# Kernel tuning notes

Hardware: AMD Instinct MI355X
Metric: run time of the kernel (lower is better)

The kernel has to match this reference:

```python
import jax, jax.numpy as jnp
import numpy as np
from jax import lax

N_HEADS = 12
HEAD_DIM = 64
ALPHA = 4.0  # spikingjelly surrogate.Sigmoid default alpha
EPS = 1e-5   # BatchNorm1d default eps

@jax.custom_vjp
def _heaviside(v):
    return (v >= 0.0).astype(v.dtype)

def _heaviside_fwd(v):
    return _heaviside(v), v

def _heaviside_bwd(v, g):
    sg = jax.nn.sigmoid(ALPHA * v)
    return (g * ALPHA * sg * (1.0 - sg),)

_heaviside.defvjp(_heaviside_fwd, _heaviside_bwd)

def if_node(x):
    """Multi-step IFNode (v_threshold=1, hard reset to 0), scan over leading T dim."""
    def step(v, xt):
        v = v + xt                      # integrate
        s = _heaviside(v - 1.0)         # fire
        v = (1.0 - s) * v               # hard reset: spiked neurons -> 0
        return v, s
    _, spikes = lax.scan(step, jnp.zeros_like(x[0]), x)
    return spikes

def bn1d(x):
    """Fresh (training-mode) BatchNorm1d over (T, S, D) with channels=S;
    affine weight=1, bias=0 at init, so pure normalization over axes (0,2)."""
    mean = x.mean(axis=(0, 2), keepdims=True)
    var = x.var(axis=(0, 2), keepdims=True)  # biased variance, as torch BN uses
    return (x - mean) * lax.rsqrt(var + EPS)

def setup_inputs() -> dict:
    key = jax.random.key(0)
    ks = jax.random.split(key, 5)
    T, S, D = 4, 2048, 768
    x = jax.random.normal(ks[0], (T, S, D), dtype=jnp.float32)
    scale = 0.02
    wq = jax.random.normal(ks[1], (D, D), dtype=jnp.float32) * scale
    wk = jax.random.normal(ks[2], (D, D), dtype=jnp.float32) * scale
    wv = jax.random.normal(ks[3], (D, D), dtype=jnp.float32) * scale
    wo = jax.random.normal(ks[4], (D, D), dtype=jnp.float32) * scale
    return {"x": x, "wq": wq, "wk": wk, "wv": wv, "wo": wo, "cur_pos": S}

def reference(x, wq, wk, wv, wo, cur_pos):
    T, S, D = x.shape
    tmp = if_node(x)                    # init_spike
    Q = tmp @ wq
    V = tmp @ wv
    K = tmp @ wk
    Q = if_node(bn1d(Q))                # spike_q(bnq(Q))
    V = if_node(bn1d(V))                # spike_v(bnv(V))
    K = if_node(bn1d(K))                # spike_k(bnk(K))
    # (T, S, H, hd) -> (T, H, S, hd)
    Qh = Q.reshape(T, S, N_HEADS, HEAD_DIM).transpose(0, 2, 1, 3)
    Vh = V.reshape(T, S, N_HEADS, HEAD_DIM).transpose(0, 2, 1, 3)
    Kh = K.reshape(T, S, N_HEADS, HEAD_DIM).transpose(0, 2, 1, 3)
    QK = (Qh * Kh).sum(axis=2, keepdims=True)   # (T, H, 1, hd)
    QK = if_node(QK)                    # talking_heads
    QKV = Vh * QK                       # (T, H, S, hd)
    QKV = QKV.transpose(0, 2, 1, 3).reshape(T, S, D)
    return bn1d(QKV @ wo)
```

## Files before the change

kernel.cpp:

```cpp
#include <hip/hip_runtime.h>

#define T_ 4
#define S_ 2048
#define D_ 768
#define SD_ (S_ * D_)
#define TSD_ (T_ * SD_)
#define H_ 12
#define HD_ 64
#define PLANE_BYTES 2359296u

typedef int int32x4 __attribute__((ext_vector_type(4)));

__device__ __forceinline__ void cp16(unsigned char* lds, const unsigned char* g) {
    __builtin_amdgcn_global_load_lds(
        (const __attribute__((address_space(1))) unsigned int*)g,
        (__attribute__((address_space(3))) unsigned int*)lds, 16, 0, 0);
}

__device__ __forceinline__ size_t frag_addr(int m, int d) {
    return ((size_t)(m >> 4) * 12 + (d >> 6)) * 1024 +
           (size_t)(((d >> 4) & 3) * 256 + (m & 15) * 16 + (d & 15));
}

__global__ __launch_bounds__(256) void k_prep_all(const float* __restrict__ wq,
                                                  const float* __restrict__ wk,
                                                  const float* __restrict__ wv,
                                                  const float* __restrict__ wo,
                                                  const float* __restrict__ x,
                                                  unsigned char* __restrict__ Bp,
                                                  unsigned char* __restrict__ Sx) {
    __shared__ unsigned char wl[4096];
    int tid = threadIdx.x;
    if (blockIdx.y < 4) {
        const float* W = (blockIdx.y == 0) ? wq : (blockIdx.y == 1) ? wk
                       : (blockIdx.y == 2) ? wv : wo;
        unsigned char* out = Bp + (size_t)blockIdx.y * PLANE_BYTES;
        int c = blockIdx.x;
        int kb = c % 12;
        int nbg = c / 12;
        int k_loc = tid >> 2;
        int n_base = (tid & 3) * 4;
        float4 w4 = *(const float4*)(
            W + (size_t)(kb * 64 + k_loc) * D_ + nbg * 16 + n_base);
        float wsv[4] = {w4.x, w4.y, w4.z, w4.w};
#pragma unroll
        for (int j = 0; j < 4; j++) {
            int n_loc = n_base + j;
            int u = (int)rintf(wsv[j] * 1073741824.0f);
#pragma unroll
            for (int p = 0; p < 4; p++) {
                wl[p * 1024 + (n_loc + 16 * (k_loc >> 4)) * 16 + (k_loc & 15)] =
                    (unsigned char)(u & 255);
                u = (u + 128) >> 8;
            }
        }
        __syncthreads();
        int p = tid >> 6;
        int lane = tid & 63;
        uint4 val = *(const uint4*)&wl[p * 1024 + lane * 16];
        *(uint4*)(out + (size_t)((p * 48 + nbg) * 12 + kb) * 1024 + lane * 16) =
            val;
    } else {
        if (blockIdx.x >= 384) return;
        int gid = blockIdx.x * 256 + tid;
        int s = gid / 48;
        int d0 = (gid % 48) * 16;
        double v[16];
#pragma unroll
        for (int j = 0; j < 16; j++) v[j] = 0.0;
#pragma unroll
        for (int t = 0; t < T_; t++) {
            union { uint4 u; unsigned char b[16]; } sp;
#pragma unroll
            for (int q = 0; q < 4; q++) {
                float4 xt = *(const float4*)(
                    x + (size_t)t * SD_ + (size_t)s * D_ + d0 + q * 4);
                float xs[4] = {xt.x, xt.y, xt.z, xt.w};
#pragma unroll
                for (int j = 0; j < 4; j++) {
                    int jj = q * 4 + j;
                    v[jj] += (double)xs[j];
                    unsigned char ss = (v[jj] >= 1.0) ? 1 : 0;
                    sp.b[jj] = ss;
                    if (ss) v[jj] = 0.0;
                }
            }
            *(uint4*)(Sx + frag_addr(t * S_ + s, d0)) = sp.u;
        }
    }
}

__global__ __launch_bounds__(256, 2) void k_gemm_i8(
    const unsigned char* __restrict__ A,
    const unsigned char* __restrict__ Bp,
    const unsigned char* __restrict__ Ms,
    float* __restrict__ C0, float* __restrict__ C1, float* __restrict__ C2,
    int bzoff) {
    int z = blockIdx.z;
    const unsigned char* B = Bp + (size_t)(bzoff + z) * PLANE_BYTES;
    float* C = (z == 0) ? C0 : (z == 1) ? C1 : C2;

    __shared__ __align__(16) unsigned char bsm[2 * 16384];

    int tid = threadIdx.x;
    int lane = tid & 63;
    int w = tid >> 6;
    int wm = w >> 1;
    int wn = w & 1;
    int row0 = blockIdx.x * 128;
    int tI = row0 >> 11;
    int n0 = blockIdx.y * 64;
    int nbg0 = blockIdx.y * 4;
    int col = lane & 15;
    int quad = lane >> 4;

    int32x4 zerov = {0, 0, 0, 0};
    int32x4 acc[4][2][4];
#pragma unroll
    for (int mb = 0; mb < 4; mb++)
#pragma unroll
        for (int nb = 0; nb < 2; nb++)
#pragma unroll
            for (int p = 0; p < 4; p++) acc[mb][nb][p] = zerov;

    const unsigned char* Ab =
        A + (size_t)((row0 >> 4) + wm * 4) * 12 * 1024 + lane * 16;

    auto stageB = [&](int buf, int kb) {
        unsigned char* bb = bsm + buf * 16384;
#pragma unroll
        for (int qi = 0; qi < 4; qi++) {
            int q = w * 4 + qi;
            int p = q >> 2, nb = q & 3;
            cp16(bb + q * 1024,
                 B + (size_t)((p * 48 + nbg0 + nb) * 12 + kb) * 1024 + lane * 16);
        }
    };

    int32x4 a[2][4];
#pragma unroll
    for (int mb = 0; mb < 4; mb++)
        a[0][mb] = *(const int32x4*)(Ab + (size_t)(mb * 12) * 1024);
    stageB(0, 0);
    __syncthreads();

    for (int kb = 0; kb < 12; kb++) {
        int cur = kb & 1;
        if (kb < 11) {
            stageB(1 - cur, kb + 1);
#pragma unroll
            for (int mb = 0; mb < 4; mb++)
                a[1 - cur][mb] = *(const int32x4*)(
                    Ab + (size_t)(mb * 12 + kb + 1) * 1024);
        }
        int32x4 af[4];
#pragma unroll
        for (int mb = 0; mb < 4; mb++) af[mb] = a[cur][mb];
        if (Ms) {
            int32x4 mv = *(const int32x4*)(Ms + tI * D_ + kb * 64 + quad * 16);
#pragma unroll
            for (int mb = 0; mb < 4; mb++) af[mb] &= mv;
        }
        const unsigned char* bb = bsm + cur * 16384;
#pragma unroll
        for (int p = 0; p < 4; p++)
#pragma unroll
            for (int nb = 0; nb < 2; nb++) {
                int32x4 bf = *(const int32x4*)(
                    bb + (size_t)(p * 4 + wn * 2 + nb) * 1024 + lane * 16);
#pragma unroll
                for (int mb = 0; mb < 4; mb++)
                    acc[mb][nb][p] = __builtin_amdgcn_mfma_i32_16x16x64_i8(
                        af[mb], bf, acc[mb][nb][p], 0, 0, 0);
            }
        __syncthreads();
    }

#pragma unroll
    for (int mb = 0; mb < 4; mb++)
#pragma unroll
        for (int nb = 0; nb < 2; nb++)
#pragma unroll
            for (int r = 0; r < 4; r++) {
                long t = (long)acc[mb][nb][0][r] + ((long)acc[mb][nb][1][r] << 8)
                       + ((long)acc[mb][nb][2][r] << 16)
                       + ((long)acc[mb][nb][3][r] << 24);
                float v = (float)((double)t * (1.0 / 1073741824.0));
                int rr = row0 + wm * 64 + mb * 16 + quad * 4 + r;
                int cc = n0 + wn * 32 + nb * 16 + col;
                C[(size_t)rr * D_ + cc] = v;
            }
}

__global__ __launch_bounds__(256) void k_bn_if(const float* __restrict__ Qf,
                                               const float* __restrict__ Kf,
                                               const float* __restrict__ Vf,
                                               unsigned char* __restrict__ Qs,
                                               unsigned char* __restrict__ Ks,
                                               unsigned char* __restrict__ Vs) {
    int s = blockIdx.x;
    int y = blockIdx.y;
    const float* X = (y == 0) ? Qf : (y == 1) ? Kf : Vf;
    unsigned char* Sp = (y == 0) ? Qs : (y == 1) ? Ks : Vs;

    __shared__ float buf[T_][D_];
    __shared__ double red[16];
    __shared__ unsigned char spk[T_ * D_];

    int tid = threadIdx.x;
    double sum = 0.0, sumsq = 0.0;
#pragma unroll
    for (int t = 0; t < T_; t++) {
        for (int d = tid; d < D_; d += 256) {
            float v = X[(size_t)t * SD_ + (size_t)s * D_ + d];
            buf[t][d] = v;
            double dv = (double)v;
            sum += dv;
            sumsq += dv * dv;
        }
    }
#pragma unroll
    for (int off = 32; off > 0; off >>= 1) {
        sum += __shfl_down(sum, off);
        sumsq += __shfl_down(sumsq, off);
    }
    int lane = tid & 63, wv = tid >> 6;
    if (lane == 0) { red[wv] = sum; red[4 + wv] = sumsq; }
    __syncthreads();
    if (tid == 0) {
        double s4 = red[0] + red[1] + red[2] + red[3];
        double q4 = red[4] + red[5] + red[6] + red[7];
        double mean = s4 / 3072.0;
        double var = q4 / 3072.0 - mean * mean;
        red[8] = mean;
        red[9] = 1.0 / sqrt(var + 1e-5);
    }
    __syncthreads();
    double mean = red[8], rstd = red[9];
    for (int d = tid; d < D_; d += 256) {
        double v = 0.0;
#pragma unroll
        for (int t = 0; t < T_; t++) {
            double xn = ((double)buf[t][d] - mean) * rstd;
            v += xn;
            int sp = (v >= 1.0) ? 1 : 0;
            spk[t * D_ + d] = (unsigned char)sp;
            if (sp) v = 0.0;
        }
    }
    __syncthreads();
    if (tid < 192) {
        int tt = tid / 48, gg = tid % 48;
        uint4 val = *(const uint4*)&spk[tt * D_ + gg * 16];
        size_t dst = ((size_t)(tt * 128 + (s >> 4)) * 12 + (gg >> 2)) * 1024 +
                     (size_t)((gg & 3) * 256 + (s & 15) * 16);
        *(uint4*)(Sp + dst) = val;
    }
}

__global__ __launch_bounds__(256) void k_qk(const unsigned char* __restrict__ Qs,
                                            const unsigned char* __restrict__ Ks,
                                            float* __restrict__ QK) {
    int t = blockIdx.x / H_;
    int h = blockIdx.x % H_;
    int lane = threadIdx.x & 63;
    int w = threadIdx.x >> 6;
    size_t base = ((size_t)t * 128 * 12 + h) * 1024 + lane * 16;
    uint4 acc = make_uint4(0, 0, 0, 0);
    for (int c = w; c < 128; c += 4) {
        uint4 q = *(const uint4*)(Qs + base + (size_t)c * 12288);
        uint4 k = *(const uint4*)(Ks + base + (size_t)c * 12288);
        acc.x += q.x & k.x;
        acc.y += q.y & k.y;
        acc.z += q.z & k.z;
        acc.w += q.w & k.w;
    }
    __shared__ unsigned int part[4][64][4];
    part[w][lane][0] = acc.x;
    part[w][lane][1] = acc.y;
    part[w][lane][2] = acc.z;
    part[w][lane][3] = acc.w;
    __syncthreads();
    if (threadIdx.x < 64) {
        int quad = threadIdx.x >> 4;
        int rem = threadIdx.x & 15;
        int dw = rem >> 2;
        int b = rem & 3;
        unsigned int tot = 0;
#pragma unroll
        for (int ww = 0; ww < 4; ww++)
            for (int cc = 0; cc < 16; cc++)
                tot += (part[ww][quad * 16 + cc][dw] >> (8 * b)) & 255u;
        QK[t * D_ + h * HD_ + quad * 16 + dw * 4 + b] = (float)tot;
    }
}

__global__ __launch_bounds__(256) void k_if_qk(const float* __restrict__ QK,
                                               unsigned char* __restrict__ QKm) {
    int j = blockIdx.x * 256 + threadIdx.x;
    if (j >= D_) return;
    float v = 0.f;
#pragma unroll
    for (int t = 0; t < T_; t++) {
        v += QK[t * D_ + j];
        unsigned char sp = (v >= 1.0f) ? 1 : 0;
        QKm[t * D_ + j] = sp;
        if (sp) v = 0.f;
    }
}

__global__ __launch_bounds__(256) void k_bn_out(const float* __restrict__ Xin,
                                                float* __restrict__ out) {
    int s = blockIdx.x;
    __shared__ float buf[T_][D_];
    __shared__ double red[16];
    int tid = threadIdx.x;
    double sum = 0.0, sumsq = 0.0;
#pragma unroll
    for (int t = 0; t < T_; t++) {
        for (int d = tid; d < D_; d += 256) {
            float v = Xin[(size_t)t * SD_ + (size_t)s * D_ + d];
            buf[t][d] = v;
            double dv = (double)v;
            sum += dv;
            sumsq += dv * dv;
        }
    }
#pragma unroll
    for (int off = 32; off > 0; off >>= 1) {
        sum += __shfl_down(sum, off);
        sumsq += __shfl_down(sumsq, off);
    }
    int lane = tid & 63, wv = tid >> 6;
    if (lane == 0) { red[wv] = sum; red[4 + wv] = sumsq; }
    __syncthreads();
    if (tid == 0) {
        double s4 = red[0] + red[1] + red[2] + red[3];
        double q4 = red[4] + red[5] + red[6] + red[7];
        double mean = s4 / 3072.0;
        double var = q4 / 3072.0 - mean * mean;
        red[8] = mean;
        red[9] = 1.0 / sqrt(var + 1e-5);
    }
    __syncthreads();
    double mean = red[8], rstd = red[9];
    for (int d = tid; d < D_; d += 256) {
#pragma unroll
        for (int t = 0; t < T_; t++) {
            double v = (double)buf[t][d];
            out[(size_t)t * SD_ + (size_t)s * D_ + d] =
                (float)((v - mean) * rstd);
        }
    }
}

extern "C" void kernel_launch(void* const* d_in, const int* in_sizes, int n_in,
                              void* d_out, int out_size, void* d_ws,
                              size_t ws_size, hipStream_t stream) {
    const float* x  = (const float*)d_in[0];
    const float* wq = (const float*)d_in[1];
    const float* wk = (const float*)d_in[2];
    const float* wv = (const float*)d_in[3];
    const float* wo = (const float*)d_in[4];
    float* out = (float*)d_out;

    float* ws  = (float*)d_ws;
    float* Qf  = ws;
    float* Kf  = ws + (size_t)TSD_;
    float* Vf  = ws + (size_t)2 * TSD_;
    float* QK  = ws + (size_t)3 * TSD_;
    unsigned char* QKm = (unsigned char*)(QK + T_ * D_);
    unsigned char* Sx  = QKm + 4096;
    unsigned char* Ks  = Sx + (size_t)TSD_;
    unsigned char* Vs  = Ks + (size_t)TSD_;
    unsigned char* Bp  = Vs + (size_t)TSD_;
    unsigned char* Qs  = Sx;

    k_prep_all<<<dim3(576, 5), 256, 0, stream>>>(wq, wk, wv, wo, x, Bp, Sx);
    k_gemm_i8<<<dim3(64, 12, 3), 256, 0, stream>>>(Sx, Bp, nullptr,
                                                   Qf, Kf, Vf, 0);
    k_bn_if<<<dim3(S_, 3), 256, 0, stream>>>(Qf, Kf, Vf, Qs, Ks, Vs);
    k_qk<<<T_ * H_, 256, 0, stream>>>(Qs, Ks, QK);
    k_if_qk<<<3, 256, 0, stream>>>(QK, QKm);
    k_gemm_i8<<<dim3(64, 12, 1), 256, 0, stream>>>(Vs, Bp, QKm, Qf, Qf, Qf, 3);
    k_bn_out<<<S_, 256, 0, stream>>>(Qf, out);
}
```

Baseline: 246.5 us.

## Fuse BN+IF for Q/K/V with QK spike-mask reduction via atomicOr bitmask

Replaces the separate BN+IF, QK reduction and talking-heads IF kernels with one kernel per sequence position. It normalizes and spikes Q, K and V together and OR-reduces the Q&K spikes into a packed mask with atomicOr. This is exact because a count of at least 1 always fires the IF node and resets it. The change avoids writing and re-reading the Q/K spike planes, drops two launches, and zeroes the mask buffer inside the prep kernel. The int8 GEMM also stages two K-blocks per barrier, which halves the syncs but doubles LDS use. Its epilogue combines partial sums in double instead of int64.

```diff
diff --git a/kernel.cpp b/kernel.cpp
--- a/kernel.cpp
+++ b/kernel.cpp
@@ -28,7 +28,8 @@
                                                   const float* __restrict__ wo,
                                                   const float* __restrict__ x,
                                                   unsigned char* __restrict__ Bp,
-                                                  unsigned char* __restrict__ Sx) {
+                                                  unsigned char* __restrict__ Sx,
+                                                  unsigned int* __restrict__ QKp) {
     __shared__ unsigned char wl[4096];
     int tid = threadIdx.x;
     if (blockIdx.y < 4) {
@@ -61,7 +62,13 @@
         *(uint4*)(out + (size_t)((p * 48 + nbg) * 12 + kb) * 1024 + lane * 16) =
             val;
     } else {
-        if (blockIdx.x >= 384) return;
+        if (blockIdx.x >= 384) {
+            if (blockIdx.x < 432) {
+                int idx = (blockIdx.x - 384) * 256 + tid;
+                QKp[idx] = 0u;
+            }
+            return;
+        }
         int gid = blockIdx.x * 256 + tid;
         int s = gid / 48;
         int d0 = (gid % 48) * 16;
@@ -93,14 +100,15 @@
 __global__ __launch_bounds__(256, 2) void k_gemm_i8(
     const unsigned char* __restrict__ A,
     const unsigned char* __restrict__ Bp,
-    const unsigned char* __restrict__ Ms,
+    const unsigned int* __restrict__ Mp,
     float* __restrict__ C0, float* __restrict__ C1, float* __restrict__ C2,
     int bzoff) {
     int z = blockIdx.z;
     const unsigned char* B = Bp + (size_t)(bzoff + z) * PLANE_BYTES;
     float* C = (z == 0) ? C0 : (z == 1) ? C1 : C2;
 
-    __shared__ __align__(16) unsigned char bsm[2 * 16384];
+    __shared__ __align__(16) unsigned char bsm[2 * 32768];
+    __shared__ __align__(16) unsigned int maskw[192];
 
     int tid = threadIdx.x;
     int lane = tid & 63;
@@ -126,53 +134,67 @@
     const unsigned char* Ab =
         A + (size_t)((row0 >> 4) + wm * 4) * 12 * 1024 + lane * 16;
 
-    auto stageB = [&](int buf, int kb) {
-        unsigned char* bb = bsm + buf * 16384;
-#pragma unroll
-        for (int qi = 0; qi < 4; qi++) {
-            int q = w * 4 + qi;
-            int p = q >> 2, nb = q & 3;
-            cp16(bb + q * 1024,
-                 B + (size_t)((p * 48 + nbg0 + nb) * 12 + kb) * 1024 + lane * 16);
-        }
+    auto stageB = [&](int buf, int kb2) {
+        unsigned char* bb = bsm + buf * 32768;
+#pragma unroll
+        for (int kk = 0; kk < 2; kk++)
+#pragma unroll
+            for (int qi = 0; qi < 4; qi++) {
+                int q = w * 4 + qi;
+                int p = q >> 2, nb = q & 3;
+                cp16(bb + kk * 16384 + q * 1024,
+                     B + (size_t)((p * 48 + nbg0 + nb) * 12 + 2 * kb2 + kk) *
+                             1024 + lane * 16);
+            }
     };
 
+    stageB(0, 0);
+    if (Mp && tid < 192) {
+        unsigned int m = 0;
+#pragma unroll
+        for (int c = 0; c < 16; c++) m |= Mp[c * 768 + tI * 192 + tid];
+        maskw[tid] = m;
+    }
     int32x4 a[2][4];
 #pragma unroll
     for (int mb = 0; mb < 4; mb++)
         a[0][mb] = *(const int32x4*)(Ab + (size_t)(mb * 12) * 1024);
-    stageB(0, 0);
     __syncthreads();
 
-    for (int kb = 0; kb < 12; kb++) {
-        int cur = kb & 1;
-        if (kb < 11) {
-            stageB(1 - cur, kb + 1);
-#pragma unroll
-            for (int mb = 0; mb < 4; mb++)
-                a[1 - cur][mb] = *(const int32x4*)(
-                    Ab + (size_t)(mb * 12 + kb + 1) * 1024);
-        }
-        int32x4 af[4];
-#pragma unroll
-        for (int mb = 0; mb < 4; mb++) af[mb] = a[cur][mb];
-        if (Ms) {
-            int32x4 mv = *(const int32x4*)(Ms + tI * D_ + kb * 64 + quad * 16);
-#pragma unroll
-            for (int mb = 0; mb < 4; mb++) af[mb] &= mv;
-        }
-        const unsigned char* bb = bsm + cur * 16384;
-#pragma unroll
-        for (int p = 0; p < 4; p++)
-#pragma unroll
-            for (int nb = 0; nb < 2; nb++) {
-                int32x4 bf = *(const int32x4*)(
-                    bb + (size_t)(p * 4 + wn * 2 + nb) * 1024 + lane * 16);
+    for (int kb2 = 0; kb2 < 6; kb2++) {
+        int cur = kb2 & 1;
+        if (kb2 < 5) stageB(1 - cur, kb2 + 1);
+#pragma unroll
+        for (int kbh = 0; kbh < 2; kbh++) {
+            int kb = kb2 * 2 + kbh;
+            if (kb < 11) {
 #pragma unroll
                 for (int mb = 0; mb < 4; mb++)
-                    acc[mb][nb][p] = __builtin_amdgcn_mfma_i32_16x16x64_i8(
-                        af[mb], bf, acc[mb][nb][p], 0, 0, 0);
-            }
+                    a[(kb + 1) & 1][mb] = *(const int32x4*)(
+                        Ab + (size_t)(mb * 12 + kb + 1) * 1024);
+            }
+            int32x4 af[4];
+#pragma unroll
+            for (int mb = 0; mb < 4; mb++) af[mb] = a[kb & 1][mb];
+            if (Mp) {
+                int32x4 mv = *(const int32x4*)(
+                    (const unsigned char*)maskw + kb * 64 + quad * 16);
+#pragma unroll
+                for (int mb = 0; mb < 4; mb++) af[mb] &= mv;
+            }
+            const unsigned char* bb = bsm + cur * 32768 + kbh * 16384;
+#pragma unroll
+            for (int p = 0; p < 4; p++)
+#pragma unroll
+                for (int nb = 0; nb < 2; nb++) {
+                    int32x4 bf = *(const int32x4*)(
+                        bb + (size_t)(p * 4 + wn * 2 + nb) * 1024 + lane * 16);
+#pragma unroll
+                    for (int mb = 0; mb < 4; mb++)
+                        acc[mb][nb][p] = __builtin_amdgcn_mfma_i32_16x16x64_i8(
+                            af[mb], bf, acc[mb][nb][p], 0, 0, 0);
+                }
+        }
         __syncthreads();
     }
 
@@ -182,37 +204,111 @@
         for (int nb = 0; nb < 2; nb++)
 #pragma unroll
             for (int r = 0; r < 4; r++) {
-                long t = (long)acc[mb][nb][0][r] + ((long)acc[mb][nb][1][r] << 8)
-                       + ((long)acc[mb][nb][2][r] << 16)
-                       + ((long)acc[mb][nb][3][r] << 24);
-                float v = (float)((double)t * (1.0 / 1073741824.0));
+                double td = (double)acc[mb][nb][0][r]
+                          + 256.0 * (double)acc[mb][nb][1][r]
+                          + 65536.0 * (double)acc[mb][nb][2][r]
+                          + 16777216.0 * (double)acc[mb][nb][3][r];
+                float v = (float)(td * (1.0 / 1073741824.0));
                 int rr = row0 + wm * 64 + mb * 16 + quad * 4 + r;
                 int cc = n0 + wn * 32 + nb * 16 + col;
                 C[(size_t)rr * D_ + cc] = v;
             }
 }
 
-__global__ __launch_bounds__(256) void k_bn_if(const float* __restrict__ Qf,
-                                               const float* __restrict__ Kf,
-                                               const float* __restrict__ Vf,
-                                               unsigned char* __restrict__ Qs,
-                                               unsigned char* __restrict__ Ks,
-                                               unsigned char* __restrict__ Vs) {
+__global__ __launch_bounds__(256) void k_bnif_qk(const float* __restrict__ Qf,
+                                                 const float* __restrict__ Kf,
+                                                 const float* __restrict__ Vf,
+                                                 unsigned char* __restrict__ Vs,
+                                                 unsigned int* __restrict__ QKp) {
     int s = blockIdx.x;
-    int y = blockIdx.y;
-    const float* X = (y == 0) ? Qf : (y == 1) ? Kf : Vf;
-    unsigned char* Sp = (y == 0) ? Qs : (y == 1) ? Ks : Vs;
-
+    __shared__ float buf[3][T_][D_];
+    __shared__ double red[8];
+    __shared__ unsigned char spkV[T_ * D_];
+    __shared__ unsigned char spkA[T_ * D_];
+    __shared__ double stats[3][2];
+
+    int tid = threadIdx.x;
+    const float* Xs[3] = {Qf, Kf, Vf};
+#pragma unroll
+    for (int y = 0; y < 3; y++) {
+        double sum = 0.0, sumsq = 0.0;
+#pragma unroll
+        for (int t = 0; t < T_; t++) {
+            for (int d = tid; d < D_; d += 256) {
+                float v = Xs[y][(size_t)t * SD_ + (size_t)s * D_ + d];
+                buf[y][t][d] = v;
+                double dv = (double)v;
+                sum += dv;
+                sumsq += dv * dv;
+            }
+        }
+#pragma unroll
+        for (int off = 32; off > 0; off >>= 1) {
+            sum += __shfl_down(sum, off);
+            sumsq += __shfl_down(sumsq, off);
+        }
+        int lane = tid & 63, wv = tid >> 6;
+        if (lane == 0) { red[wv] = sum; red[4 + wv] = sumsq; }
+        __syncthreads();
+        if (tid == 0) {
+            double s4 = red[0] + red[1] + red[2] + red[3];
+            double q4 = red[4] + red[5] + red[6] + red[7];
+            double mean = s4 / 3072.0;
+            double var = q4 / 3072.0 - mean * mean;
+            stats[y][0] = mean;
+            stats[y][1] = 1.0 / sqrt(var + 1e-5);
+        }
+        __syncthreads();
+    }
+
+    for (int d = tid; d < D_; d += 256) {
+        unsigned char qs[T_], ks[T_];
+#pragma unroll
+        for (int y = 0; y < 3; y++) {
+            double mean = stats[y][0], rstd = stats[y][1];
+            double v = 0.0;
+#pragma unroll
+            for (int t = 0; t < T_; t++) {
+                double xn = ((double)buf[y][t][d] - mean) * rstd;
+                v += xn;
+                unsigned char sp = (v >= 1.0) ? 1 : 0;
+                if (y == 0) qs[t] = sp;
+                else if (y == 1) ks[t] = sp;
+                else spkV[t * D_ + d] = sp;
+                if (sp) v = 0.0;
+            }
+        }
+#pragma unroll
+        for (int t = 0; t < T_; t++) spkA[t * D_ + d] = qs[t] & ks[t];
+    }
+    __syncthreads();
+
+    if (tid < 192) {
+        int tt = tid / 48, gg = tid % 48;
+        uint4 val = *(const uint4*)&spkV[tt * D_ + gg * 16];
+        size_t dst = ((size_t)(tt * 128 + (s >> 4)) * 12 + (gg >> 2)) * 1024 +
+                     (size_t)((gg & 3) * 256 + (s & 15) * 16);
+        *(uint4*)(Vs + dst) = val;
+        unsigned int* dstq = QKp + (s & 15) * 768;
+#pragma unroll
+        for (int t = 0; t < T_; t++) {
+            unsigned int word = *(const unsigned int*)&spkA[t * D_ + tid * 4];
+            if (word) atomicOr(dstq + t * 192 + tid, word);
+        }
+    }
+}
+
+__global__ __launch_bounds__(256) void k_bn_out(const float* __restrict__ Xin,
+                                                float* __restrict__ out) {
+    int s = blockIdx.x;
     __shared__ float buf[T_][D_];
     __shared__ double red[16];
-    __shared__ unsigned char spk[T_ * D_];
-
     int tid = threadIdx.x;
     double sum = 0.0, sumsq = 0.0;
 #pragma unroll
     for (int t = 0; t < T_; t++) {
         for (int d = tid; d < D_; d += 256) {
-            float v = X[(size_t)t * SD_ + (size_t)s * D_ + d];
+            float v = Xin[(size_t)t * SD_ + (size_t)s * D_ + d];
             buf[t][d] = v;
             double dv = (double)v;
             sum += dv;
@@ -238,113 +334,6 @@
     __syncthreads();
     double mean = red[8], rstd = red[9];
     for (int d = tid; d < D_; d += 256) {
-        double v = 0.0;
-#pragma unroll
-        for (int t = 0; t < T_; t++) {
-            double xn = ((double)buf[t][d] - mean) * rstd;
-            v += xn;
-            int sp = (v >= 1.0) ? 1 : 0;
-            spk[t * D_ + d] = (unsigned char)sp;
-            if (sp) v = 0.0;
-        }
-    }
-    __syncthreads();
-    if (tid < 192) {
-        int tt = tid / 48, gg = tid % 48;
-        uint4 val = *(const uint4*)&spk[tt * D_ + gg * 16];
-        size_t dst = ((size_t)(tt * 128 + (s >> 4)) * 12 + (gg >> 2)) * 1024 +
-                     (size_t)((gg & 3) * 256 + (s & 15) * 16);
-        *(uint4*)(Sp + dst) = val;
-    }
-}
-
-__global__ __launch_bounds__(256) void k_qk(const unsigned char* __restrict__ Qs,
-                                            const unsigned char* __restrict__ Ks,
-                                            float* __restrict__ QK) {
-    int t = blockIdx.x / H_;
-    int h = blockIdx.x % H_;
-    int lane = threadIdx.x & 63;
-    int w = threadIdx.x >> 6;
-    size_t base = ((size_t)t * 128 * 12 + h) * 1024 + lane * 16;
-    uint4 acc = make_uint4(0, 0, 0, 0);
-    for (int c = w; c < 128; c += 4) {
-        uint4 q = *(const uint4*)(Qs + base + (size_t)c * 12288);
-        uint4 k = *(const uint4*)(Ks + base + (size_t)c * 12288);
-        acc.x += q.x & k.x;
-        acc.y += q.y & k.y;
-        acc.z += q.z & k.z;
-        acc.w += q.w & k.w;
-    }
-    __shared__ unsigned int part[4][64][4];
-    part[w][lane][0] = acc.x;
-    part[w][lane][1] = acc.y;
-    part[w][lane][2] = acc.z;
-    part[w][lane][3] = acc.w;
-    __syncthreads();
-    if (threadIdx.x < 64) {
-        int quad = threadIdx.x >> 4;
-        int rem = threadIdx.x & 15;
-        int dw = rem >> 2;
-        int b = rem & 3;
-        unsigned int tot = 0;
-#pragma unroll
-        for (int ww = 0; ww < 4; ww++)
-            for (int cc = 0; cc < 16; cc++)
-                tot += (part[ww][quad * 16 + cc][dw] >> (8 * b)) & 255u;
-        QK[t * D_ + h * HD_ + quad * 16 + dw * 4 + b] = (float)tot;
-    }
-}
-
-__global__ __launch_bounds__(256) void k_if_qk(const float* __restrict__ QK,
-                                               unsigned char* __restrict__ QKm) {
-    int j = blockIdx.x * 256 + threadIdx.x;
-    if (j >= D_) return;
-    float v = 0.f;
-#pragma unroll
-    for (int t = 0; t < T_; t++) {
-        v += QK[t * D_ + j];
-        unsigned char sp = (v >= 1.0f) ? 1 : 0;
-        QKm[t * D_ + j] = sp;
-        if (sp) v = 0.f;
-    }
-}
-
-__global__ __launch_bounds__(256) void k_bn_out(const float* __restrict__ Xin,
-                                                float* __restrict__ out) {
-    int s = blockIdx.x;
-    __shared__ float buf[T_][D_];
-    __shared__ double red[16];
-    int tid = threadIdx.x;
-    double sum = 0.0, sumsq = 0.0;
-#pragma unroll
-    for (int t = 0; t < T_; t++) {
-        for (int d = tid; d < D_; d += 256) {
-            float v = Xin[(size_t)t * SD_ + (size_t)s * D_ + d];
-            buf[t][d] = v;
-            double dv = (double)v;
-            sum += dv;
-            sumsq += dv * dv;
-        }
-    }
-#pragma unroll
-    for (int off = 32; off > 0; off >>= 1) {
-        sum += __shfl_down(sum, off);
-        sumsq += __shfl_down(sumsq, off);
-    }
-    int lane = tid & 63, wv = tid >> 6;
-    if (lane == 0) { red[wv] = sum; red[4 + wv] = sumsq; }
-    __syncthreads();
-    if (tid == 0) {
-        double s4 = red[0] + red[1] + red[2] + red[3];
-        double q4 = red[4] + red[5] + red[6] + red[7];
-        double mean = s4 / 3072.0;
-        double var = q4 / 3072.0 - mean * mean;
-        red[8] = mean;
-        red[9] = 1.0 / sqrt(var + 1e-5);
-    }
-    __syncthreads();
-    double mean = red[8], rstd = red[9];
-    for (int d = tid; d < D_; d += 256) {
 #pragma unroll
         for (int t = 0; t < T_; t++) {
             double v = (double)buf[t][d];
@@ -368,20 +357,16 @@
     float* Qf  = ws;
     float* Kf  = ws + (size_t)TSD_;
     float* Vf  = ws + (size_t)2 * TSD_;
-    float* QK  = ws + (size_t)3 * TSD_;
-    unsigned char* QKm = (unsigned char*)(QK + T_ * D_);
-    unsigned char* Sx  = QKm + 4096;
-    unsigned char* Ks  = Sx + (size_t)TSD_;
-    unsigned char* Vs  = Ks + (size_t)TSD_;
-    unsigned char* Bp  = Vs + (size_t)TSD_;
-    unsigned char* Qs  = Sx;
-
-    k_prep_all<<<dim3(576, 5), 256, 0, stream>>>(wq, wk, wv, wo, x, Bp, Sx);
+    unsigned int* QKp = (unsigned int*)(ws + (size_t)3 * TSD_);
+    unsigned char* Sx = (unsigned char*)(QKp + 12288);
+    unsigned char* Vs = Sx + (size_t)TSD_;
+    unsigned char* Bp = Vs + (size_t)TSD_;
+
+    k_prep_all<<<dim3(576, 5), 256, 0, stream>>>(wq, wk, wv, wo, x, Bp, Sx,
+                                                 QKp);
     k_gemm_i8<<<dim3(64, 12, 3), 256, 0, stream>>>(Sx, Bp, nullptr,
                                                    Qf, Kf, Vf, 0);
-    k_bn_if<<<dim3(S_, 3), 256, 0, stream>>>(Qf, Kf, Vf, Qs, Ks, Vs);
-    k_qk<<<T_ * H_, 256, 0, stream>>>(Qs, Ks, QK);
-    k_if_qk<<<3, 256, 0, stream>>>(QK, QKm);
-    k_gemm_i8<<<dim3(64, 12, 1), 256, 0, stream>>>(Vs, Bp, QKm, Qf, Qf, Qf, 3);
+    k_bnif_qk<<<S_, 256, 0, stream>>>(Qf, Kf, Vf, Vs, QKp);
+    k_gemm_i8<<<dim3(64, 12, 1), 256, 0, stream>>>(Vs, Bp, QKp, Qf, Qf, Qf, 3);
     k_bn_out<<<S_, 256, 0, stream>>>(Qf, out);
 }
```

Result: faster. 227.7 us (-7.6%).
